# Kernel tuning notes

Hardware: AMD Instinct MI355X
Metric: run time of the kernel (lower is better)

## Reference

```python
import jax, jax.numpy as jnp
import numpy as np

DEPTH, B, H, E = 4, 4096, 1024, 1024  # embedDim == h so all layers stack


def setup_inputs() -> dict:
    key = jax.random.key(0)
    k1, k2, k3, k4 = jax.random.split(key, 4)
    x = jax.random.normal(k1, (B, E), dtype=jnp.float32)
    s_h = jax.random.normal(k2, (DEPTH, B, H), dtype=jnp.float32)
    s_c = jax.random.normal(k3, (DEPTH, B, H), dtype=jnp.float32)
    # Linear(embedDim + h, 4h) per layer; stored as [in, out] (transposed torch layout)
    W = jax.random.normal(k4, (DEPTH, E + H, 4 * H), dtype=jnp.float32) * 0.02
    b = jnp.zeros((DEPTH, 4 * H), dtype=jnp.float32)
    return {"x": x, "s_h": s_h, "s_c": s_c, "W": W, "b": b}


def _lstm_layer(out, layer_params):
    hh, c, Wl, bl = layer_params
    xh = jnp.concatenate([out, hh], axis=1)          # [B, E+H]
    z = xh @ Wl + bl                                  # [B, 4H]
    i, f, o, g = jnp.split(z, 4, axis=1)              # torch.split(Wx, h, 1) order: i,f,o,g
    i = jax.nn.sigmoid(i)
    f = jax.nn.sigmoid(f)
    o = jax.nn.sigmoid(o)
    g = jnp.tanh(g)
    # trainable=False -> no dropout on g
    c_new = c * f + g * i
    h_new = jnp.tanh(c_new) * o
    return h_new, (h_new, c_new)


def reference(x, s_h, s_c, W, b):
    # scan over depth: layer l consumes previous layer's output as its input
    out, (h_new, c_new) = jax.lax.scan(_lstm_layer, x, (s_h, s_c, W, b))
    return out, h_new, c_new
```

## Files before the change

### kernel.cpp

```cpp
#include <hip/hip_runtime.h>
#include <hip/hip_bf16.h>
#include <stdint.h>

#define DEPTH 4
#define Bb 4096
#define Hh 1024
#define Ee 1024
#define Kd 2048
#define Ng 4096
#define NT (Kd / 64)

typedef __attribute__((ext_vector_type(8))) short short8;
typedef __attribute__((ext_vector_type(4))) float floatx4;
typedef __attribute__((ext_vector_type(4))) float f32x4;

__device__ __forceinline__ float fast_sigmoid(float x) {
  return 1.0f / (1.0f + __expf(-x));
}
__device__ __forceinline__ float fast_tanh(float x) {
  float t = __expf(-2.0f * fabsf(x));
  return copysignf((1.0f - t) / (1.0f + t), x);
}

__device__ __forceinline__ void gload_lds16(const void* g, void* l) {
  __builtin_amdgcn_global_load_lds(
      (const __attribute__((address_space(1))) void*)(uintptr_t)g,
      (__attribute__((address_space(3))) void*)(uint32_t)(uintptr_t)l,
      16, 0, 0);
}

__global__ __launch_bounds__(256) void transpose_w_kernel(
    const float* __restrict__ W, __hip_bfloat16* __restrict__ Wt) {
  __shared__ __attribute__((aligned(16))) float ldsT[64 * 132];
  const int l = blockIdx.z;
  const int k0 = blockIdx.x * 128;
  const int n0 = blockIdx.y * 64;
  const float* Wl = W + (size_t)l * Kd * Ng + (size_t)k0 * Ng + n0;
  __hip_bfloat16* Wtl = Wt + (size_t)l * Ng * Kd;
  const int tid = threadIdx.x;

#pragma unroll
  for (int i = 0; i < 8; i++) {
    const int flat = tid + 256 * i;
    const int k = flat >> 4;
    const int c4 = (flat & 15) * 4;
    const f32x4 v = *(const f32x4*)(Wl + (size_t)k * Ng + c4);
    const int grp = k >> 3;
    const int klo = k & 7;
#pragma unroll
    for (int j = 0; j < 4; j++) {
      const int n = c4 + j;
      ldsT[n * 132 + ((grp ^ ((n >> 2) & 3)) << 3) + klo] = v[j];
    }
  }
  __syncthreads();

#pragma unroll
  for (int i = 0; i < 4; i++) {
    const int c = tid + 256 * i;
    const int n = c >> 4;
    const int kc = c & 15;
    const int g = kc ^ ((n >> 2) & 3);
    const float* src = &ldsT[n * 132 + (g << 3)];
    const f32x4 u0 = *(const f32x4*)src;
    const f32x4 u1 = *(const f32x4*)(src + 4);
    union {
      __hip_bfloat16 h[8];
      short8 s;
    } p;
    p.h[0] = __float2bfloat16(u0.x);
    p.h[1] = __float2bfloat16(u0.y);
    p.h[2] = __float2bfloat16(u0.z);
    p.h[3] = __float2bfloat16(u0.w);
    p.h[4] = __float2bfloat16(u1.x);
    p.h[5] = __float2bfloat16(u1.y);
    p.h[6] = __float2bfloat16(u1.z);
    p.h[7] = __float2bfloat16(u1.w);
    *(short8*)&Wtl[(size_t)(n0 + n) * Kd + k0 + kc * 8] = p.s;
  }
}

__global__ __launch_bounds__(256) void prefill_xh_kernel(
    const float* __restrict__ x, const float* __restrict__ s_h,
    __hip_bfloat16* __restrict__ xh) {
  const int idx = blockIdx.x * blockDim.x + threadIdx.x;
  const int XN = Bb * Ee / 4;
  const int TOTAL = XN + DEPTH * Bb * Hh / 4;
  if (idx >= TOTAL) return;
  const float* srcp;
  __hip_bfloat16* dst;
  if (idx < XN) {
    const int b = idx >> 8;
    const int j4 = idx & 255;
    srcp = x + (size_t)idx * 4;
    dst = xh + (size_t)b * Kd + j4 * 4;
  } else {
    const int e4 = idx - XN;
    const int l = e4 >> 20;
    const int r = e4 & 0xFFFFF;
    const int b = r >> 8;
    const int j4 = r & 255;
    srcp = s_h + (size_t)e4 * 4;
    dst = xh + (size_t)l * Bb * Kd + (size_t)b * Kd + Ee + j4 * 4;
  }
  f32x4 v = *(const f32x4*)srcp;
  union {
    __hip_bfloat16 h[4];
    unsigned long long u;
  } p;
  p.h[0] = __float2bfloat16(v.x);
  p.h[1] = __float2bfloat16(v.y);
  p.h[2] = __float2bfloat16(v.z);
  p.h[3] = __float2bfloat16(v.w);
  *(unsigned long long*)dst = p.u;
}

__global__ __launch_bounds__(512, 2) void lstm_layer_kernel(
    const __hip_bfloat16* __restrict__ A, const __hip_bfloat16* __restrict__ Wt,
    const float* __restrict__ bias, const float* __restrict__ c_in,
    float* __restrict__ out_h, float* __restrict__ out_c,
    float* __restrict__ out_final, __hip_bfloat16* __restrict__ xh_next) {
  __shared__ __attribute__((aligned(16))) __hip_bfloat16 sm[4 * 256 * 64];

  const int tid = threadIdx.x;
  const int lane = tid & 63;
  const int wave = tid >> 6;
  const int wm = wave >> 2;
  const int wn = wave & 3;
  const int m0 = blockIdx.y * 256;
  const int j0 = blockIdx.x * 64;

  const int r0 = tid >> 3;
  const int p = tid & 7;
  const int q = p ^ (r0 & 7);
  const __hip_bfloat16* aSrc[2][2];
  const __hip_bfloat16* bSrc[2][2];
#pragma unroll
  for (int h = 0; h < 2; h++)
#pragma unroll
    for (int i = 0; i < 2; i++) {
      const int r = r0 + i * 64;
      const int ar = m0 + h * 128 + r;
      aSrc[h][i] = A + (size_t)ar * Kd + q * 8;
      const int tr = h * 128 + r;
      const int nrow = (tr >> 6) * Hh + j0 + (tr & 63);
      bSrc[h][i] = Wt + (size_t)nrow * Kd + q * 8;
    }

#define STAGEA(h, kt, buf)                                                  \
  do {                                                                      \
    __hip_bfloat16* _d = sm + (buf) * 16384 + (h) * 8192 + tid * 8;         \
    gload_lds16(aSrc[h][0] + (kt) * 64, _d);                                \
    gload_lds16(aSrc[h][1] + (kt) * 64, _d + 4096);                         \
  } while (0)
#define STAGEB(h, kt, buf)                                                  \
  do {                                                                      \
    __hip_bfloat16* _d = sm + 32768 + (buf) * 16384 + (h) * 8192 + tid * 8; \
    gload_lds16(bSrc[h][0] + (kt) * 64, _d);                                \
    gload_lds16(bSrc[h][1] + (kt) * 64, _d + 4096);                         \
  } while (0)

  const int qk = lane >> 4;
  const int lm = lane & 15;
  const int pc0 = qk ^ (lm & 7);
  const int pc1 = (4 + qk) ^ (lm & 7);
  const int aBase = (wm * 128 + lm) * 64;
  const int bBase = (wn * 16 + lm) * 64;

  floatx4 acc[8][4];
#pragma unroll
  for (int mi = 0; mi < 8; mi++)
#pragma unroll
    for (int g = 0; g < 4; g++) acc[mi][g] = floatx4{0.f, 0.f, 0.f, 0.f};

  STAGEA(0, 0, 0);
  STAGEA(1, 0, 0);
  STAGEB(0, 0, 0);
  STAGEB(1, 0, 0);
  STAGEA(0, 1, 1);
  STAGEA(1, 1, 1);
  STAGEB(0, 1, 1);
  asm volatile("s_waitcnt vmcnt(6)" ::: "memory");
  __builtin_amdgcn_sched_barrier(0);
  __builtin_amdgcn_s_barrier();

  for (int t = 0; t < NT; ++t) {
    const int cur = t & 1;
    const __hip_bfloat16* As_c = sm + cur * 16384;
    const __hip_bfloat16* Bs_c = sm + 32768 + cur * 16384;

    short8 af[8][2];
    short8 bfg[2];

#pragma unroll
    for (int mi = 0; mi < 8; mi++) {
      af[mi][0] = *(const short8*)&As_c[aBase + mi * 1024 + pc0 * 8];
      af[mi][1] = *(const short8*)&As_c[aBase + mi * 1024 + pc1 * 8];
    }
    bfg[0] = *(const short8*)&Bs_c[bBase + pc0 * 8];
    bfg[1] = *(const short8*)&Bs_c[bBase + pc1 * 8];
    if (t + 1 < NT) STAGEB(1, t + 1, cur ^ 1);
    __builtin_amdgcn_s_barrier();
    asm volatile("s_waitcnt lgkmcnt(0)" ::: "memory");
    __builtin_amdgcn_sched_barrier(0);
    __builtin_amdgcn_s_setprio(1);
#pragma unroll
    for (int mi = 0; mi < 8; mi++) {
      acc[mi][0] = __builtin_amdgcn_mfma_f32_16x16x32_bf16(af[mi][0], bfg[0],
                                                           acc[mi][0], 0, 0, 0);
      acc[mi][0] = __builtin_amdgcn_mfma_f32_16x16x32_bf16(af[mi][1], bfg[1],
                                                           acc[mi][0], 0, 0, 0);
    }
    __builtin_amdgcn_s_setprio(0);
    __builtin_amdgcn_s_barrier();

#pragma unroll
    for (int g = 1; g < 4; g++) {
      bfg[0] = *(const short8*)&Bs_c[bBase + g * 4096 + pc0 * 8];
      bfg[1] = *(const short8*)&Bs_c[bBase + g * 4096 + pc1 * 8];
      if (t + 2 < NT) {
        if (g == 1)
          STAGEA(0, t + 2, cur);
        else if (g == 2)
          STAGEA(1, t + 2, cur);
        else
          STAGEB(0, t + 2, cur);
      }
      __builtin_amdgcn_s_barrier();
      asm volatile("s_waitcnt lgkmcnt(0)" ::: "memory");
      __builtin_amdgcn_sched_barrier(0);
      __builtin_amdgcn_s_setprio(1);
#pragma unroll
      for (int mi = 0; mi < 8; mi++) {
        acc[mi][g] = __builtin_amdgcn_mfma_f32_16x16x32_bf16(
            af[mi][0], bfg[0], acc[mi][g], 0, 0, 0);
        acc[mi][g] = __builtin_amdgcn_mfma_f32_16x16x32_bf16(
            af[mi][1], bfg[1], acc[mi][g], 0, 0, 0);
      }
      __builtin_amdgcn_s_setprio(0);
      if (g < 3) {
        __builtin_amdgcn_s_barrier();
      } else {
        if (t < NT - 2)
          asm volatile("s_waitcnt vmcnt(6)" ::: "memory");
        else
          asm volatile("s_waitcnt vmcnt(0)" ::: "memory");
        __builtin_amdgcn_sched_barrier(0);
        __builtin_amdgcn_s_barrier();
      }
    }
  }

  const int j = j0 + wn * 16 + lm;
  const float bi = bias[j];
  const float bf_ = bias[Hh + j];
  const float bo = bias[2 * Hh + j];
  const float bg = bias[3 * Hh + j];
#pragma unroll
  for (int mi = 0; mi < 8; mi++) {
    const int row0 = m0 + wm * 128 + mi * 16 + qk * 4;
#pragma unroll
    for (int r = 0; r < 4; r++) {
      const int row = row0 + r;
      const float zi = acc[mi][0][r] + bi;
      const float zf = acc[mi][1][r] + bf_;
      const float zo = acc[mi][2][r] + bo;
      const float zg = acc[mi][3][r] + bg;
      const float ig = fast_sigmoid(zi);
      const float fg = fast_sigmoid(zf);
      const float og = fast_sigmoid(zo);
      const float gg = fast_tanh(zg);
      const float c = c_in[(size_t)row * Hh + j];
      const float cn = fmaf(c, fg, gg * ig);
      const float hn = fast_tanh(cn) * og;
      out_h[(size_t)row * Hh + j] = hn;
      out_c[(size_t)row * Hh + j] = cn;
      if (xh_next) xh_next[(size_t)row * Kd + j] = __float2bfloat16(hn);
      if (out_final) out_final[(size_t)row * Hh + j] = hn;
    }
  }
#undef STAGEA
#undef STAGEB
}

extern "C" void kernel_launch(void* const* d_in, const int* in_sizes, int n_in,
                              void* d_out, int out_size, void* d_ws,
                              size_t ws_size, hipStream_t stream) {
  const float* x = (const float*)d_in[0];
  const float* s_h = (const float*)d_in[1];
  const float* s_c = (const float*)d_in[2];
  const float* W = (const float*)d_in[3];
  const float* bias = (const float*)d_in[4];
  float* out = (float*)d_out;

  __hip_bfloat16* Wt = (__hip_bfloat16*)d_ws;
  __hip_bfloat16* xh =
      (__hip_bfloat16*)((char*)d_ws + (size_t)DEPTH * Ng * Kd * 2);

  transpose_w_kernel<<<dim3(Kd / 128, Ng / 64, DEPTH), 256, 0, stream>>>(W, Wt);
  prefill_xh_kernel<<<(Bb * Ee / 4 + DEPTH * Bb * Hh / 4) / 256, 256, 0,
                      stream>>>(x, s_h, xh);

  float* out_h = out + (size_t)Bb * Ee;
  float* out_c = out_h + (size_t)DEPTH * Bb * Hh;
  for (int l = 0; l < DEPTH; l++) {
    lstm_layer_kernel<<<dim3(Hh / 64, Bb / 256), 512, 0, stream>>>(
        xh + (size_t)l * Bb * Kd, Wt + (size_t)l * Ng * Kd,
        bias + (size_t)l * Ng, s_c + (size_t)l * Bb * Hh,
        out_h + (size_t)l * Bb * Hh, out_c + (size_t)l * Bb * Hh,
        (l == DEPTH - 1) ? out : nullptr,
        (l < DEPTH - 1) ? xh + (size_t)(l + 1) * Bb * Kd : nullptr);
  }
}
```

Baseline: 660.6 us.

## Restructure K-loop into two phases with all B fragments preloaded

Each K-tile iteration now loads all A and B fragments for the four gates up front. It then runs MFMAs for gates 0-1, issues the next-next-tile global-to-LDS loads after a single barrier, and runs MFMAs for gates 2-3. This replaces the earlier four-phase schedule, which had a barrier per gate, to cut barrier count and give longer MFMA runs between syncs. Source pointers are also reduced from eight precomputed addresses to two bases with offsets, which lowers register use. In exchange, more B fragment registers are live at once, which may raise VGPR pressure at two blocks per CU of 512 threads.

Measured after the change: 654.1 us. No clear change (-1.0%).

```diff
diff --git a/kernel.cpp b/kernel.cpp
--- a/kernel.cpp
+++ b/kernel.cpp
@@ -133,31 +133,22 @@
   const int r0 = tid >> 3;
   const int p = tid & 7;
   const int q = p ^ (r0 & 7);
-  const __hip_bfloat16* aSrc[2][2];
-  const __hip_bfloat16* bSrc[2][2];
-#pragma unroll
-  for (int h = 0; h < 2; h++)
-#pragma unroll
-    for (int i = 0; i < 2; i++) {
-      const int r = r0 + i * 64;
-      const int ar = m0 + h * 128 + r;
-      aSrc[h][i] = A + (size_t)ar * Kd + q * 8;
-      const int tr = h * 128 + r;
-      const int nrow = (tr >> 6) * Hh + j0 + (tr & 63);
-      bSrc[h][i] = Wt + (size_t)nrow * Kd + q * 8;
-    }
-
-#define STAGEA(h, kt, buf)                                                  \
-  do {                                                                      \
-    __hip_bfloat16* _d = sm + (buf) * 16384 + (h) * 8192 + tid * 8;         \
-    gload_lds16(aSrc[h][0] + (kt) * 64, _d);                                \
-    gload_lds16(aSrc[h][1] + (kt) * 64, _d + 4096);                         \
+  const __hip_bfloat16* aS = A + (size_t)(m0 + r0) * Kd + q * 8;
+  const __hip_bfloat16* bS = Wt + (size_t)(j0 + r0) * Kd + q * 8;
+
+#define STAGEA(h, kt, buf)                                          \
+  do {                                                              \
+    __hip_bfloat16* _d = sm + (buf) * 16384 + (h) * 8192 + tid * 8; \
+    gload_lds16(aS + (size_t)((h) * 128) * Kd + (kt) * 64, _d);     \
+    gload_lds16(aS + (size_t)((h) * 128 + 64) * Kd + (kt) * 64,     \
+                _d + 4096);                                         \
   } while (0)
 #define STAGEB(h, kt, buf)                                                  \
   do {                                                                      \
     __hip_bfloat16* _d = sm + 32768 + (buf) * 16384 + (h) * 8192 + tid * 8; \
-    gload_lds16(bSrc[h][0] + (kt) * 64, _d);                                \
-    gload_lds16(bSrc[h][1] + (kt) * 64, _d + 4096);                         \
+    gload_lds16(bS + (size_t)((h) * 2) * 1024 * Kd + (kt) * 64, _d);        \
+    gload_lds16(bS + (size_t)((h) * 2 + 1) * 1024 * Kd + (kt) * 64,         \
+                _d + 4096);                                                 \
   } while (0)
 
   const int qk = lane >> 4;
@@ -190,65 +181,70 @@
     const __hip_bfloat16* Bs_c = sm + 32768 + cur * 16384;
 
     short8 af[8][2];
-    short8 bfg[2];
-
-#pragma unroll
-    for (int mi = 0; mi < 8; mi++) {
+    short8 bfg[4][2];
+
+#pragma unroll
+    for (int mi = 0; mi < 4; mi++) {
       af[mi][0] = *(const short8*)&As_c[aBase + mi * 1024 + pc0 * 8];
       af[mi][1] = *(const short8*)&As_c[aBase + mi * 1024 + pc1 * 8];
     }
-    bfg[0] = *(const short8*)&Bs_c[bBase + pc0 * 8];
-    bfg[1] = *(const short8*)&Bs_c[bBase + pc1 * 8];
+#pragma unroll
+    for (int g = 0; g < 2; g++) {
+      bfg[g][0] = *(const short8*)&Bs_c[bBase + g * 4096 + pc0 * 8];
+      bfg[g][1] = *(const short8*)&Bs_c[bBase + g * 4096 + pc1 * 8];
+    }
     if (t + 1 < NT) STAGEB(1, t + 1, cur ^ 1);
-    __builtin_amdgcn_s_barrier();
+#pragma unroll
+    for (int mi = 4; mi < 8; mi++) {
+      af[mi][0] = *(const short8*)&As_c[aBase + mi * 1024 + pc0 * 8];
+      af[mi][1] = *(const short8*)&As_c[aBase + mi * 1024 + pc1 * 8];
+    }
+#pragma unroll
+    for (int g = 2; g < 4; g++) {
+      bfg[g][0] = *(const short8*)&Bs_c[bBase + g * 4096 + pc0 * 8];
+      bfg[g][1] = *(const short8*)&Bs_c[bBase + g * 4096 + pc1 * 8];
+    }
+
+    __builtin_amdgcn_s_setprio(1);
+#pragma unroll
+    for (int mi = 0; mi < 8; mi++)
+#pragma unroll
+      for (int g = 0; g < 2; g++) {
+        acc[mi][g] = __builtin_amdgcn_mfma_f32_16x16x32_bf16(
+            af[mi][0], bfg[g][0], acc[mi][g], 0, 0, 0);
+        acc[mi][g] = __builtin_amdgcn_mfma_f32_16x16x32_bf16(
+            af[mi][1], bfg[g][1], acc[mi][g], 0, 0, 0);
+      }
+    __builtin_amdgcn_s_setprio(0);
+
     asm volatile("s_waitcnt lgkmcnt(0)" ::: "memory");
     __builtin_amdgcn_sched_barrier(0);
+    __builtin_amdgcn_s_barrier();
+
+    if (t + 2 < NT) {
+      STAGEA(0, t + 2, cur);
+      STAGEA(1, t + 2, cur);
+      STAGEB(0, t + 2, cur);
+    }
+
     __builtin_amdgcn_s_setprio(1);
 #pragma unroll
-    for (int mi = 0; mi < 8; mi++) {
-      acc[mi][0] = __builtin_amdgcn_mfma_f32_16x16x32_bf16(af[mi][0], bfg[0],
-                                                           acc[mi][0], 0, 0, 0);
-      acc[mi][0] = __builtin_amdgcn_mfma_f32_16x16x32_bf16(af[mi][1], bfg[1],
-                                                           acc[mi][0], 0, 0, 0);
-    }
+    for (int mi = 0; mi < 8; mi++)
+#pragma unroll
+      for (int g = 2; g < 4; g++) {
+        acc[mi][g] = __builtin_amdgcn_mfma_f32_16x16x32_bf16(
+            af[mi][0], bfg[g][0], acc[mi][g], 0, 0, 0);
+        acc[mi][g] = __builtin_amdgcn_mfma_f32_16x16x32_bf16(
+            af[mi][1], bfg[g][1], acc[mi][g], 0, 0, 0);
+      }
     __builtin_amdgcn_s_setprio(0);
+
+    if (t < NT - 2)
+      asm volatile("s_waitcnt vmcnt(6)" ::: "memory");
+    else
+      asm volatile("s_waitcnt vmcnt(0)" ::: "memory");
+    __builtin_amdgcn_sched_barrier(0);
     __builtin_amdgcn_s_barrier();
-
-#pragma unroll
-    for (int g = 1; g < 4; g++) {
-      bfg[0] = *(const short8*)&Bs_c[bBase + g * 4096 + pc0 * 8];
-      bfg[1] = *(const short8*)&Bs_c[bBase + g * 4096 + pc1 * 8];
-      if (t + 2 < NT) {
-        if (g == 1)
-          STAGEA(0, t + 2, cur);
-        else if (g == 2)
-          STAGEA(1, t + 2, cur);
-        else
-          STAGEB(0, t + 2, cur);
-      }
-      __builtin_amdgcn_s_barrier();
-      asm volatile("s_waitcnt lgkmcnt(0)" ::: "memory");
-      __builtin_amdgcn_sched_barrier(0);
-      __builtin_amdgcn_s_setprio(1);
-#pragma unroll
-      for (int mi = 0; mi < 8; mi++) {
-        acc[mi][g] = __builtin_amdgcn_mfma_f32_16x16x32_bf16(
-            af[mi][0], bfg[0], acc[mi][g], 0, 0, 0);
-        acc[mi][g] = __builtin_amdgcn_mfma_f32_16x16x32_bf16(
-            af[mi][1], bfg[1], acc[mi][g], 0, 0, 0);
-      }
-      __builtin_amdgcn_s_setprio(0);
-      if (g < 3) {
-        __builtin_amdgcn_s_barrier();
-      } else {
-        if (t < NT - 2)
-          asm volatile("s_waitcnt vmcnt(6)" ::: "memory");
-        else
-          asm volatile("s_waitcnt vmcnt(0)" ::: "memory");
-        __builtin_amdgcn_sched_barrier(0);
-        __builtin_amdgcn_s_barrier();
-      }
-    }
   }
 
   const int j = j0 + wn * 16 + lm;
```
